# Optimization experiments

Measured on AMD Instinct MI355X. Metric: run time of the kernel, lower is better.

## Reference

```python
import jax, jax.numpy as jnp
import numpy as np

B, C, H, W, NCH = 2, 256, 48, 48, 12


def setup_inputs() -> dict:
    key = jax.random.key(0)
    k1, k2, k3, k4, k5 = jax.random.split(key, 5)
    gray_feature = jax.random.normal(k1, (B, C, H, W), jnp.float32)
    rgb_feature = jax.random.normal(k2, (B, C, H, W), jnp.float32)
    rgb_image = jax.random.uniform(k3, (B, 3, H, W), jnp.float32)
    # one-hot segmentation labels: random class id per pixel in [0, NCH)
    gcls = jax.random.randint(k4, (B, H, W), 0, NCH)
    rcls = jax.random.randint(k5, (B, H, W), 0, NCH)
    gray_label = jax.nn.one_hot(gcls, NCH, axis=1, dtype=jnp.float32)
    rgb_label = jax.nn.one_hot(rcls, NCH, axis=1, dtype=jnp.float32)
    return dict(gray_feature=gray_feature, rgb_feature=rgb_feature,
                rgb_image=rgb_image, gray_label=gray_label, rgb_label=rgb_label)


def _masked_normalize(feat, maskf):
    # feat: [b,c,N], maskf: [b,N] in {0,1}. Subtract per-channel masked mean,
    # then divide each masked pixel's feature vector by its channel-norm.
    cnt = maskf.sum(-1)                                            # [b]
    mean = jnp.einsum('bcn,bn->bc', feat, maskf) / jnp.maximum(cnt, 1.0)[:, None]
    bar = (feat - mean[:, :, None]) * maskf[:, None, :]            # zero outside mask
    norm = jnp.sqrt(jnp.sum(bar * bar, axis=1))                    # [b,N]
    unit = bar / jnp.where(norm > 0, norm, 1.0)[:, None, :]
    return unit, cnt


def reference(gray_feature, rgb_feature, rgb_image, gray_label, rgb_label):
    b, c, h, w = gray_feature.shape
    N = h * w
    gf = gray_feature.reshape(b, c, N)
    rf = rgb_feature.reshape(b, c, N)
    img = rgb_image.reshape(b, 3, N)
    gms = gray_label.reshape(b, -1, N) > 0.5   # [b,NCH,N] bool
    rms = rgb_label.reshape(b, -1, N) > 0.5
    canvas = -jnp.ones((b, 3, N), gray_feature.dtype)
    NEG = jnp.asarray(-1e30, gray_feature.dtype)
    for k in range(1, 12):  # classes 1..11, matching the torch loop
        gm = gms[:, k]                                     # [b,N]
        rm = rms[:, k]
        gmf = gm.astype(gf.dtype)
        rmf = rm.astype(rf.dtype)
        gn, cg = _masked_normalize(gf, gmf)                # [b,c,N]
        rn, cr = _masked_normalize(rf, rmf)
        # normalized correlation between gray and rgb masked pixels
        corr = jnp.einsum('bci,bcj->bij', gn, rn)          # [b,N,N]
        logits = jnp.where(rm[:, None, :], corr, NEG)      # softmax over rgb-mask pixels
        sm = jax.nn.softmax(logits, axis=-1)
        out = jnp.einsum('bij,bcj->bci', sm, img)          # [b,3,N]
        # skip condition from torch: needs >=2 pixels on each side
        valid = (cg > 1) & (cr > 1)                        # [b]
        write = gm & valid[:, None]                        # [b,N]
        canvas = jnp.where(write[:, None, :], out, canvas)
    return canvas.reshape(b, 3, h, w)
```

## Files before the change

kernel.cpp:

```cpp
#include <hip/hip_runtime.h>
#include <math.h>

#define BN 2
#define CC 256
#define NN 2304
#define KK 12
#define MC 320
#define QT 8
#define KTL 128
#define KCH 32

#define OFF_CNT_G   0
#define OFF_CNT_R   32
#define OFF_IDX_G   64
#define OFF_CPS_G   (OFF_IDX_G + BN * KK * MC)
#define OFF_CPS_R   (OFF_CPS_G + BN * NN)
#define OFF_MSUM_G  (OFF_CPS_R + BN * NN)
#define OFF_MSUM_R  (OFF_MSUM_G + BN * KK * CC)
#define OFF_IMGC    (OFF_MSUM_R + BN * KK * CC)
#define OFF_INV_G   (OFF_IMGC + BN * KK * 3 * MC)
#define OFF_INV_R   (OFF_INV_G + BN * KK * MC)
#define OFF_UCG     (OFF_INV_R + BN * KK * MC)
#define OFF_UCR     (OFF_UCG + BN * KK * MC * CC)

__global__ __launch_bounds__(256) void prep_mean_kernel(
        const float* __restrict__ gf, const float* __restrict__ rf,
        const float* __restrict__ img, const float* __restrict__ gl,
        const float* __restrict__ rl, float* __restrict__ out,
        int* cnt_g, int* cnt_r, int* idx_g, int* cps_g, int* cps_r,
        float* imgc, float* inv_g, float* inv_r,
        float* msum_g, float* msum_r) {
    __shared__ int wcnt[4];
    __shared__ float wsum[4][KK];
    int bid = blockIdx.x, tid = threadIdx.x;
    int lane = tid & 63, wid = tid >> 6;

    if (bid < 48) {
        int type = bid / (BN * KK);
        int rem = bid % (BN * KK);
        int b = rem / KK, k = rem % KK;
        const float* lp = (type ? rl : gl) + ((size_t)(b * KK + k)) * NN;
        int* cps = type ? cps_r : cps_g;
        int* cnt = type ? cnt_r : cnt_g;
        int base = 0;
        for (int c0 = 0; c0 < NN; c0 += 256) {
            int i = c0 + tid;
            bool p = lp[i] > 0.5f;
            unsigned long long m = __ballot(p);
            int rank = __popcll(m & ((1ull << lane) - 1));
            if (lane == 0) wcnt[wid] = __popcll(m);
            __syncthreads();
            int pre = 0;
            for (int w = 0; w < wid; ++w) pre += wcnt[w];
            int tot = wcnt[0] + wcnt[1] + wcnt[2] + wcnt[3];
            if (p) {
                int pos = base + pre + rank;
                cps[b * NN + i] = (k << 16) | pos;
                if (pos < MC) {
                    if (type) {
                        for (int ch = 0; ch < 3; ++ch)
                            imgc[((b * KK + k) * 3 + ch) * MC + pos] =
                                img[((size_t)(b * 3 + ch)) * NN + i];
                    } else {
                        idx_g[(b * KK + k) * MC + pos] = i;
                    }
                }
            }
            base += tot;
            __syncthreads();
        }
        if (tid == 0) cnt[b * KK + k] = base;
        int start = base < MC ? base : MC;
        for (int pos = start + tid; pos < MC; pos += 256) {
            if (type) {
                for (int ch = 0; ch < 3; ++ch)
                    imgc[((b * KK + k) * 3 + ch) * MC + pos] = 0.f;
            } else {
                idx_g[(b * KK + k) * MC + pos] = 0;
            }
        }
        float* invc = type ? inv_r : inv_g;
        for (int pos = tid; pos < MC; pos += 256)
            invc[(b * KK + k) * MC + pos] = 0.f;
    } else {
        int u = bid - 48;
        if (u < 54) out[u * 256 + tid] = -1.0f;
        int type = u >> 9;
        int rem = u & 511;
        int b = rem >> 8, c = rem & 255;
        const float* f = (type ? rf : gf) + ((size_t)(b * CC + c)) * NN;
        const float* lab = (type ? rl : gl) + ((size_t)b) * KK * NN;
        float* msum = type ? msum_r : msum_g;

        float acc[KK];
        #pragma unroll
        for (int kk = 0; kk < KK; ++kk) acc[kk] = 0.f;
        for (int i = tid; i < NN; i += 256) {
            float v = f[i];
            #pragma unroll
            for (int kk = 0; kk < KK; ++kk) acc[kk] += lab[(size_t)kk * NN + i] * v;
        }
        #pragma unroll
        for (int kk = 0; kk < KK; ++kk) {
            #pragma unroll
            for (int o = 32; o; o >>= 1) acc[kk] += __shfl_xor(acc[kk], o, 64);
        }
        if (lane == 0) {
            #pragma unroll
            for (int kk = 0; kk < KK; ++kk) wsum[wid][kk] = acc[kk];
        }
        __syncthreads();
        if (tid < KK)
            msum[(b * KK + tid) * CC + c] =
                wsum[0][tid] + wsum[1][tid] + wsum[2][tid] + wsum[3][tid];
    }
}

__global__ __launch_bounds__(256) void center_kernel(
        const float* __restrict__ gf, const float* __restrict__ rf,
        const int* __restrict__ cps_g, const int* __restrict__ cps_r,
        const int* __restrict__ cnt_g, const int* __restrict__ cnt_r,
        const float* __restrict__ msum_g, const float* __restrict__ msum_r,
        float* ucg, float* ucr, float* inv_g, float* inv_r) {
    const int PCH = NN / 32;
    int blk = blockIdx.x;
    int type = blk / (BN * PCH);
    int rem = blk % (BN * PCH);
    int b = rem / PCH, chunk = rem % PCH;
    int i0 = chunk * 32;
    const float* f = type ? rf : gf;
    const int* cps = type ? cps_r : cps_g;
    const int* cnt = type ? cnt_r : cnt_g;
    const float* msum = type ? msum_r : msum_g;
    float* uc = type ? ucr : ucg;
    float* invc = type ? inv_r : inv_g;

    __shared__ float lmean[KK * 257];
    __shared__ float tile[64 * 33];

    int tid = threadIdx.x;
    for (int x = tid; x < KK * CC; x += 256) {
        int k = x >> 8, c = x & 255;
        float cn = fmaxf((float)cnt[b * KK + k], 1.f);
        lmean[k * 257 + c] = msum[(b * KK + k) * CC + c] / cn;
    }
    int p = tid >> 3, q = tid & 7;
    int pl = tid & 31, cb = tid >> 5;
    int kcpos = cps[b * NN + i0 + p];
    int kc = kcpos >> 16, pos = kcpos & 0xFFFF;
    bool wr = pos < MC;
    float ss = 0.f;
    float* ub = uc + ((size_t)((b * KK + kc) * MC + (wr ? pos : MC - 1))) * CC;
    for (int cc = 0; cc < 4; ++cc) {
        __syncthreads();
        for (int j = 0; j < 8; ++j) {
            int c = cb * 8 + j;
            tile[c * 33 + pl] = f[((size_t)(b * CC + cc * 64 + c)) * NN + i0 + pl];
        }
        __syncthreads();
        #pragma unroll
        for (int h = 0; h < 2; ++h) {
            int c0 = q * 8 + h * 4;
            float4 v;
            v.x = tile[(c0 + 0) * 33 + p] - lmean[kc * 257 + cc * 64 + c0 + 0];
            v.y = tile[(c0 + 1) * 33 + p] - lmean[kc * 257 + cc * 64 + c0 + 1];
            v.z = tile[(c0 + 2) * 33 + p] - lmean[kc * 257 + cc * 64 + c0 + 2];
            v.w = tile[(c0 + 3) * 33 + p] - lmean[kc * 257 + cc * 64 + c0 + 3];
            ss += v.x * v.x + v.y * v.y + v.z * v.z + v.w * v.w;
            if (wr) *(float4*)&ub[cc * 64 + c0] = v;
        }
    }
    ss += __shfl_xor(ss, 1, 64);
    ss += __shfl_xor(ss, 2, 64);
    ss += __shfl_xor(ss, 4, 64);
    if (q == 0 && wr)
        invc[(b * KK + kc) * MC + pos] = (ss > 0.f) ? rsqrtf(ss) : 1.0f;
}

__global__ __launch_bounds__(256) void corr_out_kernel(
        const int* __restrict__ cnt_g, const int* __restrict__ cnt_r,
        const int* __restrict__ idx_g,
        const float* __restrict__ ucg, const float* __restrict__ ucr,
        const float* __restrict__ inv_g, const float* __restrict__ inv_r,
        const float* __restrict__ imgc, float* __restrict__ out) {
    const int TNQ = MC / QT;
    int tq = blockIdx.x % TNQ;
    int k = (blockIdx.x / TNQ) % KK;
    int b = blockIdx.x / (TNQ * KK);
    if (k == 0) return;
    int bk = b * KK + k;
    int cg_ = cnt_g[bk], cr_ = cnt_r[bk];
    if (cg_ <= 1 || cr_ <= 1) return;
    int Mg = min(cg_, MC), Mr = min(cr_, MC);
    int q0 = tq * QT;
    if (q0 >= Mg) return;

    __shared__ float Af[QT * (CC + 4)];
    __shared__ float Bs[KCH * (KTL + 4)];

    int tid = threadIdx.x;
    {
        int r = tid >> 5, c32 = tid & 31;
        int rowi = q0 + r; if (rowi > MC - 1) rowi = MC - 1;
        const float* rowA = ucg + ((size_t)(bk * MC + rowi)) * CC;
        #pragma unroll
        for (int j = 0; j < 2; ++j) {
            int c0 = c32 * 8 + j * 4;
            *(float4*)&Af[r * (CC + 4) + c0] = *(const float4*)&rowA[c0];
        }
    }

    int ty = tid >> 5;
    int tx = tid & 31;
    int rowg = q0 + ty; if (rowg > MC - 1) rowg = MC - 1;
    float invi = inv_g[bk * MC + rowg];
    const float* im0 = imgc + (bk * 3 + 0) * MC;
    const float* im1 = imgc + (bk * 3 + 1) * MC;
    const float* im2 = imgc + (bk * 3 + 2) * MC;
    float s = 0.f, p0 = 0.f, p1 = 0.f, p2 = 0.f;

    for (int k0 = 0; k0 < Mr; k0 += KTL) {
        float acc[4] = {0.f, 0.f, 0.f, 0.f};
        for (int kcc = 0; kcc < CC; kcc += KCH) {
            __syncthreads();
            {
                int col = tid >> 1, half = tid & 1;
                int colr = k0 + col; if (colr > MC - 1) colr = MC - 1;
                const float* rowB = ucr + ((size_t)(bk * MC + colr)) * CC + kcc + half * 16;
                #pragma unroll
                for (int j = 0; j < 4; ++j) {
                    float4 vb = *(const float4*)&rowB[j * 4];
                    int c = half * 16 + j * 4;
                    Bs[(c + 0) * (KTL + 4) + col] = vb.x;
                    Bs[(c + 1) * (KTL + 4) + col] = vb.y;
                    Bs[(c + 2) * (KTL + 4) + col] = vb.z;
                    Bs[(c + 3) * (KTL + 4) + col] = vb.w;
                }
            }
            __syncthreads();
            #pragma unroll
            for (int kk = 0; kk < KCH; ++kk) {
                float av = Af[ty * (CC + 4) + kcc + kk];
                float4 bv = *(const float4*)&Bs[kk * (KTL + 4) + tx * 4];
                acc[0] += av * bv.x;
                acc[1] += av * bv.y;
                acc[2] += av * bv.z;
                acc[3] += av * bv.w;
            }
        }
        int kidx = k0 + tx * 4; if (kidx > MC - 4) kidx = MC - 4;
        float4 w0 = *(const float4*)&im0[kidx];
        float4 w1 = *(const float4*)&im1[kidx];
        float4 w2 = *(const float4*)&im2[kidx];
        float4 vj = *(const float4*)&inv_r[bk * MC + kidx];
        float wj0[4] = {w0.x, w0.y, w0.z, w0.w};
        float wj1[4] = {w1.x, w1.y, w1.z, w1.w};
        float wj2[4] = {w2.x, w2.y, w2.z, w2.w};
        float vjj[4] = {vj.x, vj.y, vj.z, vj.w};
        #pragma unroll
        for (int y = 0; y < 4; ++y) {
            int col = k0 + tx * 4 + y;
            float e = (col < Mr) ? __expf(acc[y] * invi * vjj[y]) : 0.f;
            s += e;
            p0 += e * wj0[y];
            p1 += e * wj1[y];
            p2 += e * wj2[y];
        }
    }
    #pragma unroll
    for (int o = 1; o <= 16; o <<= 1) {
        s  += __shfl_xor(s,  o, 64);
        p0 += __shfl_xor(p0, o, 64);
        p1 += __shfl_xor(p1, o, 64);
        p2 += __shfl_xor(p2, o, 64);
    }
    if (tx == 0) {
        int row = q0 + ty;
        if (row < Mg) {
            int gi = idx_g[bk * MC + row];
            float inv = 1.0f / s;
            out[((size_t)(b * 3 + 0)) * NN + gi] = p0 * inv;
            out[((size_t)(b * 3 + 1)) * NN + gi] = p1 * inv;
            out[((size_t)(b * 3 + 2)) * NN + gi] = p2 * inv;
        }
    }
}

extern "C" void kernel_launch(void* const* d_in, const int* in_sizes, int n_in,
                              void* d_out, int out_size, void* d_ws, size_t ws_size,
                              hipStream_t stream) {
    const float* gf  = (const float*)d_in[0];
    const float* rf  = (const float*)d_in[1];
    const float* img = (const float*)d_in[2];
    const float* gl  = (const float*)d_in[3];
    const float* rl  = (const float*)d_in[4];
    float* out = (float*)d_out;
    float* ws = (float*)d_ws;

    int*   cnt_g  = (int*)(ws + OFF_CNT_G);
    int*   cnt_r  = (int*)(ws + OFF_CNT_R);
    int*   idx_g  = (int*)(ws + OFF_IDX_G);
    int*   cps_g  = (int*)(ws + OFF_CPS_G);
    int*   cps_r  = (int*)(ws + OFF_CPS_R);
    float* msum_g = ws + OFF_MSUM_G;
    float* msum_r = ws + OFF_MSUM_R;
    float* imgc   = ws + OFF_IMGC;
    float* inv_g  = ws + OFF_INV_G;
    float* inv_r  = ws + OFF_INV_R;
    float* ucg    = ws + OFF_UCG;
    float* ucr    = ws + OFF_UCR;

    prep_mean_kernel<<<48 + 2 * BN * CC, 256, 0, stream>>>(
        gf, rf, img, gl, rl, out, cnt_g, cnt_r, idx_g, cps_g, cps_r,
        imgc, inv_g, inv_r, msum_g, msum_r);
    center_kernel<<<2 * BN * (NN / 32), 256, 0, stream>>>(
        gf, rf, cps_g, cps_r, cnt_g, cnt_r, msum_g, msum_r,
        ucg, ucr, inv_g, inv_r);
    corr_out_kernel<<<BN * KK * (MC / QT), 256, 0, stream>>>(
        cnt_g, cnt_r, idx_g, ucg, ucr, inv_g, inv_r, imgc, out);
}
```

Baseline: 117.1 us.

## Reuse label loads across four channels and widen correlation tiles to 2x4 per thread

The masked-mean part of the prep kernel now has each block handle four channels, so the twelve label values loaded per pixel are reused four times. This cuts redundant label traffic and reduces the block count. The correlation kernel now uses a 256-column key tile, with each thread computing two query rows by four columns. A is stored transposed in shared memory so a float2 read supplies both rows. Together these raise arithmetic per shared-memory load and halve the key-tile iterations, at the cost of more registers and a larger shared B buffer.

```diff
diff --git a/kernel.cpp b/kernel.cpp
--- a/kernel.cpp
+++ b/kernel.cpp
@@ -7,8 +7,10 @@
 #define KK 12
 #define MC 320
 #define QT 8
-#define KTL 128
+#define KTL 256
 #define KCH 32
+#define BPAD 260
+#define APAD 10
 
 #define OFF_CNT_G   0
 #define OFF_CNT_R   32
@@ -31,7 +33,7 @@
         float* imgc, float* inv_g, float* inv_r,
         float* msum_g, float* msum_r) {
     __shared__ int wcnt[4];
-    __shared__ float wsum[4][KK];
+    __shared__ float wsum[4][4][KK];
     int bid = blockIdx.x, tid = threadIdx.x;
     int lane = tid & 63, wid = tid >> 6;
 
@@ -85,34 +87,49 @@
     } else {
         int u = bid - 48;
         if (u < 54) out[u * 256 + tid] = -1.0f;
-        int type = u >> 9;
-        int rem = u & 511;
-        int b = rem >> 8, c = rem & 255;
-        const float* f = (type ? rf : gf) + ((size_t)(b * CC + c)) * NN;
+        int type = u >> 7;
+        int rem = u & 127;
+        int b = rem >> 6, cg = rem & 63;
+        const float* fb = (type ? rf : gf) + ((size_t)(b * CC + cg * 4)) * NN;
         const float* lab = (type ? rl : gl) + ((size_t)b) * KK * NN;
         float* msum = type ? msum_r : msum_g;
 
-        float acc[KK];
-        #pragma unroll
-        for (int kk = 0; kk < KK; ++kk) acc[kk] = 0.f;
+        float acc[4][KK];
+        #pragma unroll
+        for (int c = 0; c < 4; ++c)
+            #pragma unroll
+            for (int kk = 0; kk < KK; ++kk) acc[c][kk] = 0.f;
         for (int i = tid; i < NN; i += 256) {
-            float v = f[i];
-            #pragma unroll
-            for (int kk = 0; kk < KK; ++kk) acc[kk] += lab[(size_t)kk * NN + i] * v;
-        }
-        #pragma unroll
-        for (int kk = 0; kk < KK; ++kk) {
-            #pragma unroll
-            for (int o = 32; o; o >>= 1) acc[kk] += __shfl_xor(acc[kk], o, 64);
-        }
+            float lv[KK];
+            #pragma unroll
+            for (int kk = 0; kk < KK; ++kk) lv[kk] = lab[(size_t)kk * NN + i];
+            #pragma unroll
+            for (int c = 0; c < 4; ++c) {
+                float v = fb[(size_t)c * NN + i];
+                #pragma unroll
+                for (int kk = 0; kk < KK; ++kk) acc[c][kk] += lv[kk] * v;
+            }
+        }
+        #pragma unroll
+        for (int c = 0; c < 4; ++c)
+            #pragma unroll
+            for (int kk = 0; kk < KK; ++kk) {
+                #pragma unroll
+                for (int o = 32; o; o >>= 1)
+                    acc[c][kk] += __shfl_xor(acc[c][kk], o, 64);
+            }
         if (lane == 0) {
             #pragma unroll
-            for (int kk = 0; kk < KK; ++kk) wsum[wid][kk] = acc[kk];
+            for (int c = 0; c < 4; ++c)
+                #pragma unroll
+                for (int kk = 0; kk < KK; ++kk) wsum[wid][c][kk] = acc[c][kk];
         }
         __syncthreads();
-        if (tid < KK)
-            msum[(b * KK + tid) * CC + c] =
-                wsum[0][tid] + wsum[1][tid] + wsum[2][tid] + wsum[3][tid];
+        if (tid < 48) {
+            int c = tid / KK, kk = tid % KK;
+            float s = wsum[0][c][kk] + wsum[1][c][kk] + wsum[2][c][kk] + wsum[3][c][kk];
+            msum[(b * KK + kk) * CC + cg * 4 + c] = s;
+        }
     }
 }
 
@@ -195,93 +212,114 @@
     int q0 = tq * QT;
     if (q0 >= Mg) return;
 
-    __shared__ float Af[QT * (CC + 4)];
-    __shared__ float Bs[KCH * (KTL + 4)];
+    __shared__ float Af[CC * APAD];
+    __shared__ float Bs[KCH * BPAD];
 
     int tid = threadIdx.x;
     {
         int r = tid >> 5, c32 = tid & 31;
         int rowi = q0 + r; if (rowi > MC - 1) rowi = MC - 1;
         const float* rowA = ucg + ((size_t)(bk * MC + rowi)) * CC;
-        #pragma unroll
-        for (int j = 0; j < 2; ++j) {
-            int c0 = c32 * 8 + j * 4;
-            *(float4*)&Af[r * (CC + 4) + c0] = *(const float4*)&rowA[c0];
-        }
-    }
-
-    int ty = tid >> 5;
-    int tx = tid & 31;
-    int rowg = q0 + ty; if (rowg > MC - 1) rowg = MC - 1;
-    float invi = inv_g[bk * MC + rowg];
+        float4 v0 = *(const float4*)&rowA[c32 * 8];
+        float4 v1 = *(const float4*)&rowA[c32 * 8 + 4];
+        Af[(c32 * 8 + 0) * APAD + r] = v0.x;
+        Af[(c32 * 8 + 1) * APAD + r] = v0.y;
+        Af[(c32 * 8 + 2) * APAD + r] = v0.z;
+        Af[(c32 * 8 + 3) * APAD + r] = v0.w;
+        Af[(c32 * 8 + 4) * APAD + r] = v1.x;
+        Af[(c32 * 8 + 5) * APAD + r] = v1.y;
+        Af[(c32 * 8 + 6) * APAD + r] = v1.z;
+        Af[(c32 * 8 + 7) * APAD + r] = v1.w;
+    }
+
+    int ty = tid >> 6;
+    int lane = tid & 63;
+    int r0 = q0 + 2 * ty;
+    int r0c = (r0 > MC - 1) ? MC - 1 : r0;
+    int r1c = (r0 + 1 > MC - 1) ? MC - 1 : r0 + 1;
+    float invi0 = inv_g[bk * MC + r0c];
+    float invi1 = inv_g[bk * MC + r1c];
     const float* im0 = imgc + (bk * 3 + 0) * MC;
     const float* im1 = imgc + (bk * 3 + 1) * MC;
     const float* im2 = imgc + (bk * 3 + 2) * MC;
-    float s = 0.f, p0 = 0.f, p1 = 0.f, p2 = 0.f;
+    const float* ivr = inv_r + bk * MC;
+    float s[2] = {0.f, 0.f}, p0[2] = {0.f, 0.f}, p1[2] = {0.f, 0.f}, p2[2] = {0.f, 0.f};
 
     for (int k0 = 0; k0 < Mr; k0 += KTL) {
-        float acc[4] = {0.f, 0.f, 0.f, 0.f};
+        float acc[2][4];
+        #pragma unroll
+        for (int x = 0; x < 2; ++x)
+            #pragma unroll
+            for (int y = 0; y < 4; ++y) acc[x][y] = 0.f;
+
         for (int kcc = 0; kcc < CC; kcc += KCH) {
             __syncthreads();
             {
-                int col = tid >> 1, half = tid & 1;
-                int colr = k0 + col; if (colr > MC - 1) colr = MC - 1;
-                const float* rowB = ucr + ((size_t)(bk * MC + colr)) * CC + kcc + half * 16;
+                int cj = tid & 7;
+                int colg = tid >> 3;
                 #pragma unroll
-                for (int j = 0; j < 4; ++j) {
-                    float4 vb = *(const float4*)&rowB[j * 4];
-                    int c = half * 16 + j * 4;
-                    Bs[(c + 0) * (KTL + 4) + col] = vb.x;
-                    Bs[(c + 1) * (KTL + 4) + col] = vb.y;
-                    Bs[(c + 2) * (KTL + 4) + col] = vb.z;
-                    Bs[(c + 3) * (KTL + 4) + col] = vb.w;
+                for (int p8 = 0; p8 < 8; ++p8) {
+                    int col = colg + p8 * 32;
+                    int colr = k0 + col; if (colr > MC - 1) colr = MC - 1;
+                    float4 vb = *(const float4*)(ucr +
+                        ((size_t)(bk * MC + colr)) * CC + kcc + cj * 4);
+                    Bs[(cj * 4 + 0) * BPAD + col] = vb.x;
+                    Bs[(cj * 4 + 1) * BPAD + col] = vb.y;
+                    Bs[(cj * 4 + 2) * BPAD + col] = vb.z;
+                    Bs[(cj * 4 + 3) * BPAD + col] = vb.w;
                 }
             }
             __syncthreads();
             #pragma unroll
             for (int kk = 0; kk < KCH; ++kk) {
-                float av = Af[ty * (CC + 4) + kcc + kk];
-                float4 bv = *(const float4*)&Bs[kk * (KTL + 4) + tx * 4];
-                acc[0] += av * bv.x;
-                acc[1] += av * bv.y;
-                acc[2] += av * bv.z;
-                acc[3] += av * bv.w;
-            }
-        }
-        int kidx = k0 + tx * 4; if (kidx > MC - 4) kidx = MC - 4;
-        float4 w0 = *(const float4*)&im0[kidx];
-        float4 w1 = *(const float4*)&im1[kidx];
-        float4 w2 = *(const float4*)&im2[kidx];
-        float4 vj = *(const float4*)&inv_r[bk * MC + kidx];
+                float2 av = *(const float2*)&Af[(kcc + kk) * APAD + 2 * ty];
+                float4 bv = *(const float4*)&Bs[kk * BPAD + lane * 4];
+                acc[0][0] += av.x * bv.x; acc[0][1] += av.x * bv.y;
+                acc[0][2] += av.x * bv.z; acc[0][3] += av.x * bv.w;
+                acc[1][0] += av.y * bv.x; acc[1][1] += av.y * bv.y;
+                acc[1][2] += av.y * bv.z; acc[1][3] += av.y * bv.w;
+            }
+        }
+        int kbase = k0 + lane * 4; if (kbase > MC - 4) kbase = MC - 4;
+        float4 w0 = *(const float4*)&im0[kbase];
+        float4 w1 = *(const float4*)&im1[kbase];
+        float4 w2 = *(const float4*)&im2[kbase];
+        float4 vj = *(const float4*)&ivr[kbase];
         float wj0[4] = {w0.x, w0.y, w0.z, w0.w};
         float wj1[4] = {w1.x, w1.y, w1.z, w1.w};
         float wj2[4] = {w2.x, w2.y, w2.z, w2.w};
         float vjj[4] = {vj.x, vj.y, vj.z, vj.w};
         #pragma unroll
         for (int y = 0; y < 4; ++y) {
-            int col = k0 + tx * 4 + y;
-            float e = (col < Mr) ? __expf(acc[y] * invi * vjj[y]) : 0.f;
-            s += e;
-            p0 += e * wj0[y];
-            p1 += e * wj1[y];
-            p2 += e * wj2[y];
+            int col = k0 + lane * 4 + y;
+            bool ok = col < Mr;
+            float e0 = ok ? __expf(acc[0][y] * invi0 * vjj[y]) : 0.f;
+            float e1 = ok ? __expf(acc[1][y] * invi1 * vjj[y]) : 0.f;
+            s[0] += e0; p0[0] += e0 * wj0[y]; p1[0] += e0 * wj1[y]; p2[0] += e0 * wj2[y];
+            s[1] += e1; p0[1] += e1 * wj0[y]; p1[1] += e1 * wj1[y]; p2[1] += e1 * wj2[y];
         }
     }
     #pragma unroll
-    for (int o = 1; o <= 16; o <<= 1) {
-        s  += __shfl_xor(s,  o, 64);
-        p0 += __shfl_xor(p0, o, 64);
-        p1 += __shfl_xor(p1, o, 64);
-        p2 += __shfl_xor(p2, o, 64);
-    }
-    if (tx == 0) {
-        int row = q0 + ty;
-        if (row < Mg) {
-            int gi = idx_g[bk * MC + row];
-            float inv = 1.0f / s;
-            out[((size_t)(b * 3 + 0)) * NN + gi] = p0 * inv;
-            out[((size_t)(b * 3 + 1)) * NN + gi] = p1 * inv;
-            out[((size_t)(b * 3 + 2)) * NN + gi] = p2 * inv;
+    for (int o = 1; o <= 32; o <<= 1) {
+        #pragma unroll
+        for (int x = 0; x < 2; ++x) {
+            s[x]  += __shfl_xor(s[x],  o, 64);
+            p0[x] += __shfl_xor(p0[x], o, 64);
+            p1[x] += __shfl_xor(p1[x], o, 64);
+            p2[x] += __shfl_xor(p2[x], o, 64);
+        }
+    }
+    if (lane == 0) {
+        #pragma unroll
+        for (int x = 0; x < 2; ++x) {
+            int row = q0 + 2 * ty + x;
+            if (row < Mg) {
+                int gi = idx_g[bk * MC + row];
+                float inv = 1.0f / s[x];
+                out[((size_t)(b * 3 + 0)) * NN + gi] = p0[x] * inv;
+                out[((size_t)(b * 3 + 1)) * NN + gi] = p1[x] * inv;
+                out[((size_t)(b * 3 + 2)) * NN + gi] = p2[x] * inv;
+            }
         }
     }
 }
@@ -310,7 +348,7 @@
     float* ucg    = ws + OFF_UCG;
     float* ucr    = ws + OFF_UCR;
 
-    prep_mean_kernel<<<48 + 2 * BN * CC, 256, 0, stream>>>(
+    prep_mean_kernel<<<48 + 2 * BN * (CC / 4), 256, 0, stream>>>(
         gf, rf, img, gl, rl, out, cnt_g, cnt_r, idx_g, cps_g, cps_r,
         imgc, inv_g, inv_r, msum_g, msum_r);
     center_kernel<<<2 * BN * (NN / 32), 256, 0, stream>>>(
```

Result: faster. 114.7 us (-2.0%).
